# Kernel tuning notes

Hardware: AMD Instinct MI355X
Metric: run time of the kernel (lower is better)

Reference implementation:

```python
import jax, jax.numpy as jnp
import numpy as np

NQ, NL, QD, LD, H = 100000, 32, 384, 1024, 128
E, E_SEE, E_PRED = 1000000, 750000, 250000
N = NQ + NL
EPS = 1e-5


def _bn(x, g, b):
    # BatchNorm1d in training mode: biased batch statistics over node dim
    mu = x.mean(0)
    var = x.var(0)
    return g * (x - mu) * jax.lax.rsqrt(var + EPS) + b


def _general_conv(x, src, dst, ea, Wm, bm, We, be_):
    # PyG GeneralConv (heads=1, no attention, aggr='add', in==out -> identity skip)
    msg = x[src] @ Wm + bm + ea @ We + be_            # [E_see, H]
    agg = jax.ops.segment_sum(msg, dst, num_segments=N)
    return agg + x


def setup_inputs() -> dict:
    key = jax.random.key(0)
    ks = jax.random.split(key, 20)
    s = lambda fan_in: 1.0 / np.sqrt(fan_in)
    return {
        'query_features': jax.random.normal(ks[0], (NQ, QD), jnp.float32),
        'llm_features': jax.random.normal(ks[1], (NL, LD), jnp.float32),
        'edge_index': jax.random.randint(ks[2], (2, E), 0, N, jnp.int64 if jax.config.jax_enable_x64 else jnp.int32),
        'edge_mask': jax.random.randint(ks[3], (E_PRED,), 0, E),
        'edge_can_see': jax.random.randint(ks[4], (E_SEE,), 0, E),
        'edge_weight': jax.random.uniform(ks[5], (E, 1), jnp.float32),
        'Wq': jax.random.normal(ks[6], (QD, H), jnp.float32) * s(QD),
        'bq': jnp.zeros((H,), jnp.float32),
        'Wl': jax.random.normal(ks[7], (LD, H), jnp.float32) * s(LD),
        'bl': jnp.zeros((H,), jnp.float32),
        'W_em': jax.random.normal(ks[8], (1, 1), jnp.float32),
        'b_em': jnp.zeros((1,), jnp.float32),
        'W1m': jax.random.normal(ks[9], (H, H), jnp.float32) * s(H),
        'b1m': jnp.zeros((H,), jnp.float32),
        'W1e': jax.random.normal(ks[10], (1, H), jnp.float32),
        'b1e': jnp.zeros((H,), jnp.float32),
        'W2m': jax.random.normal(ks[11], (H, H), jnp.float32) * s(H),
        'b2m': jnp.zeros((H,), jnp.float32),
        'W2e': jax.random.normal(ks[12], (1, H), jnp.float32),
        'b2e': jnp.zeros((H,), jnp.float32),
        'g1': jnp.ones((H,), jnp.float32), 'beta1': jnp.zeros((H,), jnp.float32),
        'g2': jnp.ones((H,), jnp.float32), 'beta2': jnp.zeros((H,), jnp.float32),
    }


def reference(query_features, llm_features, edge_index, edge_mask, edge_can_see,
              edge_weight, Wq, bq, Wl, bl, W_em, b_em, W1m, b1m, W1e, b1e,
              W2m, b2m, W2e, b2e, g1, beta1, g2, beta2):
    lrelu = jax.nn.leaky_relu  # slope 0.01 (torch default)
    ei_mask = edge_index[:, edge_can_see]       # [2, E_see]
    ei_pred = edge_index[:, edge_mask]          # [2, E_pred]
    ew = lrelu(edge_weight[edge_can_see] @ W_em + b_em)  # [E_see, 1]
    # feature alignment
    x_ini = jnp.concatenate([query_features @ Wq + bq, llm_features @ Wl + bl], 0)  # [N, H]
    src, dst = ei_mask[0], ei_mask[1]
    x = lrelu(_bn(_general_conv(x_ini, src, dst, ew, W1m, b1m, W1e, b1e), g1, beta1))
    x = _bn(_general_conv(x, src, dst, ew, W2m, b2m, W2e, b2e), g2, beta2)
    edge_predict = jax.nn.sigmoid((x_ini[ei_pred[0]] * x[ei_pred[1]]).mean(-1))  # [E_pred]
    return edge_predict
```

## Files before the change

### kernel.cpp

```cpp
#include <hip/hip_runtime.h>
#include <math.h>

#define NQ 100000
#define NL 32
#define QD 384
#define LD 1024
#define H 128
#define E_TOT 1000000
#define E_SEE 750000
#define E_PRED 250000
#define NN (NQ + NL)
#define EPS 1e-5f

#define NB_SCAN ((NN + 255) / 256)
#define NB_GEMM ((NN + 127) / 128)
#define NB_XINI ((NQ + 127) / 128)

typedef __attribute__((ext_vector_type(8))) short short8;
typedef __attribute__((ext_vector_type(4))) short short4v;
typedef __attribute__((ext_vector_type(4))) float f32x4;

__device__ __forceinline__ unsigned short f2bf(float f) {
  unsigned int u = __builtin_bit_cast(unsigned int, f);
  u = (u + 0x7FFFu + ((u >> 16) & 1u)) >> 16;
  return (unsigned short)u;
}


__global__ void k_ew_hist(const int* __restrict__ ecs, const int* __restrict__ EI,
                          const float* __restrict__ ewt, const float* __restrict__ Wem,
                          const float* __restrict__ bem, float* __restrict__ ew,
                          int* __restrict__ cnt) {
  int e = blockIdx.x * 256 + threadIdx.x;
  if (e >= E_SEE) return;
  int idx = ecs[e];
  int d = EI[E_TOT + idx];
  atomicAdd(&cnt[d], 1);
  float w = ewt[idx] * Wem[0] + bem[0];
  ew[e] = w > 0.f ? w : 0.01f * w;
}

__global__ void k_scan_block(const int* __restrict__ cnt, int* __restrict__ bsum) {
  __shared__ int red[256];
  int i = blockIdx.x * 256 + threadIdx.x;
  red[threadIdx.x] = (i < NN) ? cnt[i] : 0;
  __syncthreads();
  for (int s = 128; s > 0; s >>= 1) {
    if (threadIdx.x < s) red[threadIdx.x] += red[threadIdx.x + s];
    __syncthreads();
  }
  if (threadIdx.x == 0) bsum[blockIdx.x] = red[0];
}

__global__ void k_scan_top(const int* __restrict__ bsum, int* __restrict__ boff) {
  __shared__ int buf[2][512];
  int t = threadIdx.x;
  int v = (t < NB_SCAN) ? bsum[t] : 0;
  buf[0][t] = v;
  __syncthreads();
  int src = 0;
  for (int d = 1; d < 512; d <<= 1) {
    int x = buf[src][t];
    if (t >= d) x += buf[src][t - d];
    buf[src ^ 1][t] = x;
    __syncthreads();
    src ^= 1;
  }
  if (t < NB_SCAN) boff[t] = buf[src][t] - v;
}

__global__ void k_scan_write(const int* __restrict__ cnt, const int* __restrict__ boff,
                             int* __restrict__ off) {
  __shared__ int buf[2][256];
  int t = threadIdx.x;
  int i = blockIdx.x * 256 + t;
  int v = (i < NN) ? cnt[i] : 0;
  buf[0][t] = v;
  __syncthreads();
  int src = 0;
  for (int d = 1; d < 256; d <<= 1) {
    int x = buf[src][t];
    if (t >= d) x += buf[src][t - d];
    buf[src ^ 1][t] = x;
    __syncthreads();
    src ^= 1;
  }
  if (i < NN) off[i] = boff[blockIdx.x] + buf[src][t] - v;
  if (i == 0) off[NN] = E_SEE;
}

__global__ void k_fill(const int* __restrict__ ecs, const int* __restrict__ EI,
                       const float* __restrict__ ew, const int* __restrict__ off,
                       int* __restrict__ cur, int* __restrict__ csr_src,
                       float* __restrict__ csr_ew) {
  int e = blockIdx.x * 256 + threadIdx.x;
  if (e >= E_SEE) return;
  int idx = ecs[e];
  int s = EI[idx];
  int d = EI[E_TOT + idx];
  int p = off[d] + atomicAdd(&cur[d], 1);
  csr_src[p] = s;
  csr_ew[p] = ew[e];
}


__global__ void k_prep(const float* __restrict__ Wq, const float* __restrict__ W1m,
                       const float* __restrict__ W2m,
                       unsigned short* __restrict__ Wqt, unsigned short* __restrict__ W1t,
                       unsigned short* __restrict__ W2t) {
  int i = blockIdx.x * 256 + threadIdx.x;
  const int tot1 = QD * H;
  const int tot2 = H * H;
  if (i < tot1) {
    int n = i / QD, k = i - n * QD;
    Wqt[i] = f2bf(Wq[(size_t)k * H + n]);
  } else if (i < tot1 + tot2) {
    int j = i - tot1;
    int n = j >> 7, k = j & 127;
    W1t[j] = f2bf(W1m[(size_t)k * H + n]);
  } else if (i < tot1 + 2 * tot2) {
    int j = i - tot1 - tot2;
    int n = j >> 7, k = j & 127;
    W2t[j] = f2bf(W2m[(size_t)k * H + n]);
  }
}


__global__ __launch_bounds__(128) void k_llm_part(const float* __restrict__ lf,
                                                  const float* __restrict__ Wl,
                                                  float* __restrict__ part) {
  int r = blockIdx.x >> 3;
  int s = blockIdx.x & 7;
  int t = threadIdx.x;
  int k0 = s * 128;
  float acc = 0.f;
#pragma unroll 4
  for (int k = 0; k < 128; k += 4) {
    float a0 = lf[(size_t)r * LD + k0 + k + 0];
    float a1 = lf[(size_t)r * LD + k0 + k + 1];
    float a2 = lf[(size_t)r * LD + k0 + k + 2];
    float a3 = lf[(size_t)r * LD + k0 + k + 3];
    acc = fmaf(a0, Wl[(size_t)(k0 + k + 0) * H + t], acc);
    acc = fmaf(a1, Wl[(size_t)(k0 + k + 1) * H + t], acc);
    acc = fmaf(a2, Wl[(size_t)(k0 + k + 2) * H + t], acc);
    acc = fmaf(a3, Wl[(size_t)(k0 + k + 3) * H + t], acc);
  }
  part[(size_t)blockIdx.x * 128 + t] = acc;
}

__global__ void k_llm_comb(const float* __restrict__ part, const float* __restrict__ bl,
                           float* __restrict__ XINI) {
  int i = blockIdx.x * 256 + threadIdx.x;
  if (i >= NL * H) return;
  int r = i >> 7, t = i & 127;
  float a = bl[t];
#pragma unroll
  for (int s = 0; s < 8; s++) a += part[(size_t)(r * 8 + s) * 128 + t];
  XINI[(size_t)(NQ + r) * H + t] = a;
}


__global__ __launch_bounds__(256) void k_xini(
    const float* __restrict__ qf, const unsigned short* __restrict__ Wqt,
    const float* __restrict__ bq, float* __restrict__ XINI) {
  __shared__ unsigned short sA[128][40];
  __shared__ unsigned short sB[128][40];
  int tid = threadIdx.x;
  int w = tid >> 6, lane = tid & 63;
  int l15 = lane & 15, quad = lane >> 4;
  int wr = (w >> 1) * 64, wc = (w & 1) * 64;
  int rowbase = blockIdx.x * 128;
  f32x4 acc[4][4];
#pragma unroll
  for (int i = 0; i < 4; i++)
#pragma unroll
    for (int j = 0; j < 4; j++) acc[i][j] = (f32x4){0.f, 0.f, 0.f, 0.f};

  int arow = tid >> 3, akc = (tid & 7) * 4;
  int bn = tid >> 2, bk8 = (tid & 3) * 8;
  float4 pa[4];
  int4 pb[2];
#pragma unroll
  for (int p = 0; p < 4; ++p) {
    int gr = rowbase + p * 32 + arow;
    pa[p] = (gr < NQ) ? *(const float4*)&qf[(size_t)gr * QD + akc]
                      : make_float4(0.f, 0.f, 0.f, 0.f);
  }
#pragma unroll
  for (int p = 0; p < 2; ++p)
    pb[p] = *(const int4*)&Wqt[(size_t)(p * 64 + bn) * QD + bk8];

  for (int step = 0; step < 12; ++step) {
    int kb = step * 32;
#pragma unroll
    for (int p = 0; p < 4; ++p) {
      short4v b;
      b.x = (short)f2bf(pa[p].x); b.y = (short)f2bf(pa[p].y);
      b.z = (short)f2bf(pa[p].z); b.w = (short)f2bf(pa[p].w);
      *(short4v*)&sA[p * 32 + arow][akc] = b;
    }
#pragma unroll
    for (int p = 0; p < 2; ++p) *(int4*)&sB[p * 64 + bn][bk8] = pb[p];
    __syncthreads();
    if (step + 1 < 12) {
      int kn = kb + 32;
#pragma unroll
      for (int p = 0; p < 4; ++p) {
        int gr = rowbase + p * 32 + arow;
        pa[p] = (gr < NQ) ? *(const float4*)&qf[(size_t)gr * QD + kn + akc]
                          : make_float4(0.f, 0.f, 0.f, 0.f);
      }
#pragma unroll
      for (int p = 0; p < 2; ++p)
        pb[p] = *(const int4*)&Wqt[(size_t)(p * 64 + bn) * QD + kn + bk8];
    }
    short8 af[4], bfr[4];
#pragma unroll
    for (int mt = 0; mt < 4; ++mt)
      af[mt] = *(const short8*)&sA[wr + mt * 16 + l15][quad * 8];
#pragma unroll
    for (int nt = 0; nt < 4; ++nt)
      bfr[nt] = *(const short8*)&sB[wc + nt * 16 + l15][quad * 8];
#pragma unroll
    for (int mt = 0; mt < 4; ++mt)
#pragma unroll
      for (int nt = 0; nt < 4; ++nt)
        acc[mt][nt] = __builtin_amdgcn_mfma_f32_16x16x32_bf16(
            af[mt], bfr[nt], acc[mt][nt], 0, 0, 0);
    __syncthreads();
  }
#pragma unroll
  for (int nt = 0; nt < 4; ++nt) {
    int col = wc + nt * 16 + l15;
    float bias = bq[col];
#pragma unroll
    for (int mt = 0; mt < 4; ++mt) {
#pragma unroll
      for (int r = 0; r < 4; ++r) {
        int n = rowbase + wr + mt * 16 + quad * 4 + r;
        if (n < NQ) XINI[(size_t)n * H + col] = acc[mt][nt][r] + bias;
      }
    }
  }
}


template <bool TRANS>
__global__ __launch_bounds__(256) void k_seg(
    const float* __restrict__ Xin, const int* __restrict__ off,
    const int* __restrict__ csr_src, const float* __restrict__ csr_ew,
    const float* __restrict__ scale, const float* __restrict__ shift,
    unsigned short* __restrict__ S16, float* __restrict__ swsum,
    float* __restrict__ degf) {
  int w = blockIdx.x * 4 + (threadIdx.x >> 6);
  if (w >= NN) return;
  int lane = threadIdx.x & 63;
  int o0 = off[w], o1 = off[w + 1];
  float ax = 1.f, ay = 1.f, bx = 0.f, by = 0.f;
  if (TRANS) {
    float2 sc = *(const float2*)&scale[lane * 2];
    float2 sh = *(const float2*)&shift[lane * 2];
    ax = sc.x; ay = sc.y; bx = sh.x; by = sh.y;
  }
  float accx = 0.f, accy = 0.f, ews = 0.f;
  for (int k = o0; k < o1; ++k) {
    int s = csr_src[k];
    float2 v = *(const float2*)&Xin[(size_t)s * H + lane * 2];
    if (TRANS) {
      float t0 = fmaf(ax, v.x, bx); v.x = t0 > 0.f ? t0 : 0.01f * t0;
      float t1 = fmaf(ay, v.y, by); v.y = t1 > 0.f ? t1 : 0.01f * t1;
    }
    accx += v.x; accy += v.y;
    ews += csr_ew[k];
  }
  unsigned int pk = ((unsigned int)f2bf(accy) << 16) | f2bf(accx);
  *(unsigned int*)&S16[(size_t)w * H + lane * 2] = pk;
  if (lane == 0) { swsum[w] = ews; degf[w] = (float)(o1 - o0); }
}


template <bool TRANS>
__global__ __launch_bounds__(256) void k_gemm(
    const unsigned short* __restrict__ S16, const float* __restrict__ Xin,
    float* __restrict__ Xout, const unsigned short* __restrict__ Wt,
    const float* __restrict__ bm, const float* __restrict__ be,
    const float* __restrict__ We,
    const float* __restrict__ scale, const float* __restrict__ shift,
    const float* __restrict__ swsum, const float* __restrict__ degf,
    float* __restrict__ partials) {
  __shared__ unsigned short sA[128][40];
  __shared__ unsigned short sB[128][40];
  __shared__ float st[2][8][128];
  int tid = threadIdx.x;
  int w = tid >> 6, lane = tid & 63;
  int l15 = lane & 15, quad = lane >> 4;
  int wr = (w >> 1) * 64, wc = (w & 1) * 64;
  int rowbase = blockIdx.x * 128;
  f32x4 acc[4][4];
#pragma unroll
  for (int i = 0; i < 4; i++)
#pragma unroll
    for (int j = 0; j < 4; j++) acc[i][j] = (f32x4){0.f, 0.f, 0.f, 0.f};

  int arow = tid >> 1, ah = (tid & 1) * 16;
  int4 pa[2], pb[2];
  {
    int gr = rowbase + arow;
    if (gr < NN) {
      pa[0] = *(const int4*)&S16[(size_t)gr * H + ah];
      pa[1] = *(const int4*)&S16[(size_t)gr * H + ah + 8];
    } else {
      pa[0] = make_int4(0, 0, 0, 0); pa[1] = make_int4(0, 0, 0, 0);
    }
    pb[0] = *(const int4*)&Wt[(size_t)arow * H + ah];
    pb[1] = *(const int4*)&Wt[(size_t)arow * H + ah + 8];
  }
  for (int step = 0; step < 4; ++step) {
    *(int4*)&sA[arow][ah] = pa[0];
    *(int4*)&sA[arow][ah + 8] = pa[1];
    *(int4*)&sB[arow][ah] = pb[0];
    *(int4*)&sB[arow][ah + 8] = pb[1];
    __syncthreads();
    if (step + 1 < 4) {
      int kn = (step + 1) * 32;
      int gr = rowbase + arow;
      if (gr < NN) {
        pa[0] = *(const int4*)&S16[(size_t)gr * H + kn + ah];
        pa[1] = *(const int4*)&S16[(size_t)gr * H + kn + ah + 8];
      } else {
        pa[0] = make_int4(0, 0, 0, 0); pa[1] = make_int4(0, 0, 0, 0);
      }
      pb[0] = *(const int4*)&Wt[(size_t)arow * H + kn + ah];
      pb[1] = *(const int4*)&Wt[(size_t)arow * H + kn + ah + 8];
    }
    short8 af[4], bfr[4];
#pragma unroll
    for (int mt = 0; mt < 4; ++mt)
      af[mt] = *(const short8*)&sA[wr + mt * 16 + l15][quad * 8];
#pragma unroll
    for (int nt = 0; nt < 4; ++nt)
      bfr[nt] = *(const short8*)&sB[wc + nt * 16 + l15][quad * 8];
#pragma unroll
    for (int mt = 0; mt < 4; ++mt)
#pragma unroll
      for (int nt = 0; nt < 4; ++nt)
        acc[mt][nt] = __builtin_amdgcn_mfma_f32_16x16x32_bf16(
            af[mt], bfr[nt], acc[mt][nt], 0, 0, 0);
    __syncthreads();
  }
  int col4[4];
  float cb4[4], we4[4], sc4[4], sh4[4], ps[4], pq[4];
#pragma unroll
  for (int nt = 0; nt < 4; ++nt) {
    int col = wc + nt * 16 + l15;
    col4[nt] = col;
    cb4[nt] = bm[col] + be[col];
    we4[nt] = We[col];
    if (TRANS) { sc4[nt] = scale[col]; sh4[nt] = shift[col]; }
    ps[nt] = 0.f; pq[nt] = 0.f;
  }
#pragma unroll
  for (int mt = 0; mt < 4; ++mt) {
#pragma unroll
    for (int r = 0; r < 4; ++r) {
      int n = rowbase + wr + mt * 16 + quad * 4 + r;
      if (n < NN) {
        float dg = degf[n], sw = swsum[n];
#pragma unroll
        for (int nt = 0; nt < 4; ++nt) {
          float rr = Xin[(size_t)n * H + col4[nt]];
          if (TRANS) {
            float t = fmaf(sc4[nt], rr, sh4[nt]);
            rr = t > 0.f ? t : 0.01f * t;
          }
          float o = acc[mt][nt][r] + dg * cb4[nt] + sw * we4[nt] + rr;
          Xout[(size_t)n * H + col4[nt]] = o;
          ps[nt] += o; pq[nt] += o * o;
        }
      }
    }
  }
  int slot = (w >> 1) * 4 + quad;
#pragma unroll
  for (int nt = 0; nt < 4; ++nt) {
    st[0][slot][col4[nt]] = ps[nt];
    st[1][slot][col4[nt]] = pq[nt];
  }
  __syncthreads();
  int plane = tid >> 7, col = tid & 127;
  float s = 0.f;
#pragma unroll
  for (int y = 0; y < 8; y++) s += st[plane][y][col];
  partials[(size_t)blockIdx.x * 256 + tid] = s;
}


__global__ __launch_bounds__(256) void k_bnstats(
    const float* __restrict__ partials, const float* __restrict__ g,
    const float* __restrict__ beta, float* __restrict__ scale,
    float* __restrict__ shift) {
  __shared__ float rs[256], rq[256];
  int j = blockIdx.x;
  int t = threadIdx.x;
  float as = 0.f, aq = 0.f;
  for (int b = t; b < NB_GEMM; b += 256) {
    as += partials[(size_t)b * 256 + j];
    aq += partials[(size_t)b * 256 + 128 + j];
  }
  rs[t] = as; rq[t] = aq;
  __syncthreads();
  for (int s = 128; s > 0; s >>= 1) {
    if (t < s) { rs[t] += rs[t + s]; rq[t] += rq[t + s]; }
    __syncthreads();
  }
  if (t == 0) {
    float mean = rs[0] / (float)NN;
    float var = rq[0] / (float)NN - mean * mean;
    float a = g[j] * rsqrtf(var + EPS);
    scale[j] = a;
    shift[j] = beta[j] - mean * a;
  }
}


__global__ __launch_bounds__(256) void k_pred(
    const int* __restrict__ emask, const int* __restrict__ EI,
    const float* __restrict__ XINI, const float* __restrict__ X,
    const float* __restrict__ scale, const float* __restrict__ shift,
    float* __restrict__ out) {
  int i = blockIdx.x * 4 + (threadIdx.x >> 6);
  if (i >= E_PRED) return;
  int lane = threadIdx.x & 63;
  int m = emask[i];
  int p0 = EI[m];
  int p1 = EI[E_TOT + m];
  float2 a = *(const float2*)&XINI[(size_t)p0 * H + lane * 2];
  float2 b = *(const float2*)&X[(size_t)p1 * H + lane * 2];
  float2 sc = *(const float2*)&scale[lane * 2];
  float2 sh = *(const float2*)&shift[lane * 2];
  float v = a.x * fmaf(sc.x, b.x, sh.x) + a.y * fmaf(sc.y, b.y, sh.y);
#pragma unroll
  for (int mm = 32; mm > 0; mm >>= 1) v += __shfl_xor(v, mm, 64);
  if (lane == 0) out[i] = 1.f / (1.f + expf(-v * (1.f / 128.f)));
}


extern "C" void kernel_launch(void* const* d_in, const int* in_sizes, int n_in,
                              void* d_out, int out_size, void* d_ws, size_t ws_size,
                              hipStream_t stream) {
  const float* qf    = (const float*)d_in[0];
  const float* lf    = (const float*)d_in[1];
  const int*   EI    = (const int*)d_in[2];
  const int*   emask = (const int*)d_in[3];
  const int*   ecs   = (const int*)d_in[4];
  const float* ewt   = (const float*)d_in[5];
  const float* Wq    = (const float*)d_in[6];
  const float* bq    = (const float*)d_in[7];
  const float* Wl    = (const float*)d_in[8];
  const float* bl    = (const float*)d_in[9];
  const float* Wem   = (const float*)d_in[10];
  const float* bem   = (const float*)d_in[11];
  const float* W1m   = (const float*)d_in[12];
  const float* b1m   = (const float*)d_in[13];
  const float* W1e   = (const float*)d_in[14];
  const float* b1e   = (const float*)d_in[15];
  const float* W2m   = (const float*)d_in[16];
  const float* b2m   = (const float*)d_in[17];
  const float* W2e   = (const float*)d_in[18];
  const float* b2e   = (const float*)d_in[19];
  const float* g1    = (const float*)d_in[20];
  const float* beta1 = (const float*)d_in[21];
  const float* g2    = (const float*)d_in[22];
  const float* beta2 = (const float*)d_in[23];
  float* out = (float*)d_out;

  char* p = (char*)d_ws;
  auto alloc = [&](size_t bytes) -> void* {
    void* r = (void*)p;
    p += (bytes + 255) & ~(size_t)255;
    return r;
  };
  float* XINI    = (float*)alloc((size_t)NN * H * 4);
  float* X       = (float*)alloc((size_t)NN * H * 4);
  unsigned short* S16 = (unsigned short*)alloc((size_t)NN * H * 2);
  float* ew      = (float*)alloc((size_t)E_SEE * 4);
  float* csr_ew  = (float*)alloc((size_t)E_SEE * 4);
  int*   csr_src = (int*)alloc((size_t)E_SEE * 4);
  int*   cnt     = (int*)alloc((size_t)NN * 4);
  int*   off     = (int*)alloc((size_t)(NN + 1) * 4);
  int*   cur     = (int*)alloc((size_t)NN * 4);
  int*   bsum    = (int*)alloc((size_t)NB_SCAN * 4);
  int*   boff    = (int*)alloc((size_t)NB_SCAN * 4);
  float* swsum   = (float*)alloc((size_t)NN * 4);
  float* degf    = (float*)alloc((size_t)NN * 4);
  float* partials= (float*)alloc((size_t)NB_GEMM * 256 * 4);
  float* scale1  = (float*)alloc(128 * 4);
  float* shift1  = (float*)alloc(128 * 4);
  float* scale2  = (float*)alloc(128 * 4);
  float* shift2  = (float*)alloc(128 * 4);
  unsigned short* Wqt = (unsigned short*)alloc((size_t)QD * H * 2);
  unsigned short* W1t = (unsigned short*)alloc((size_t)H * H * 2);
  unsigned short* W2t = (unsigned short*)alloc((size_t)H * H * 2);
  float* llmpart = (float*)alloc((size_t)NL * 8 * H * 4);

  hipMemsetAsync(cnt, 0, (size_t)NN * 4, stream);
  hipMemsetAsync(cur, 0, (size_t)NN * 4, stream);

  int ebl = (E_SEE + 255) / 256;
  k_prep<<<320, 256, 0, stream>>>(Wq, W1m, W2m, Wqt, W1t, W2t);
  k_ew_hist<<<ebl, 256, 0, stream>>>(ecs, EI, ewt, Wem, bem, ew, cnt);
  k_scan_block<<<NB_SCAN, 256, 0, stream>>>(cnt, bsum);
  k_scan_top<<<1, 512, 0, stream>>>(bsum, boff);
  k_scan_write<<<NB_SCAN, 256, 0, stream>>>(cnt, boff, off);
  k_fill<<<ebl, 256, 0, stream>>>(ecs, EI, ew, off, cur, csr_src, csr_ew);

  k_llm_part<<<NL * 8, 128, 0, stream>>>(lf, Wl, llmpart);
  k_llm_comb<<<(NL * H + 255) / 256, 256, 0, stream>>>(llmpart, bl, XINI);
  k_xini<<<NB_XINI, 256, 0, stream>>>(qf, Wqt, bq, XINI);

  int segbl = (NN + 3) / 4;
  k_seg<false><<<segbl, 256, 0, stream>>>(XINI, off, csr_src, csr_ew,
                                          nullptr, nullptr, S16, swsum, degf);
  k_gemm<false><<<NB_GEMM, 256, 0, stream>>>(S16, XINI, X, W1t, b1m, b1e, W1e,
                                             nullptr, nullptr, swsum, degf, partials);
  k_bnstats<<<H, 256, 0, stream>>>(partials, g1, beta1, scale1, shift1);
  k_seg<true><<<segbl, 256, 0, stream>>>(X, off, csr_src, csr_ew,
                                         scale1, shift1, S16, swsum, degf);
  k_gemm<true><<<NB_GEMM, 256, 0, stream>>>(S16, X, X, W2t, b2m, b2e, W2e,
                                            scale1, shift1, swsum, degf, partials);
  k_bnstats<<<H, 256, 0, stream>>>(partials, g2, beta2, scale2, shift2);
  int pbl = (E_PRED + 3) / 4;
  k_pred<<<pbl, 256, 0, stream>>>(emask, EI, XINI, X, scale2, shift2, out);
}
```

Baseline: 722.1 us.

## Drop LDS staging in query projection GEMM, load MFMA fragments from global

```diff
diff --git a/kernel.cpp b/kernel.cpp
--- a/kernel.cpp
+++ b/kernel.cpp
@@ -19,6 +19,7 @@
 typedef __attribute__((ext_vector_type(8))) short short8;
 typedef __attribute__((ext_vector_type(4))) short short4v;
 typedef __attribute__((ext_vector_type(4))) float f32x4;
+typedef __attribute__((ext_vector_type(4))) unsigned int uint4v;
 
 __device__ __forceinline__ unsigned short f2bf(float f) {
   unsigned int u = __builtin_bit_cast(unsigned int, f);
@@ -160,85 +161,80 @@
 }
 
 
-__global__ __launch_bounds__(256) void k_xini(
+__global__ __launch_bounds__(256, 3) void k_xini(
     const float* __restrict__ qf, const unsigned short* __restrict__ Wqt,
     const float* __restrict__ bq, float* __restrict__ XINI) {
-  __shared__ unsigned short sA[128][40];
-  __shared__ unsigned short sB[128][40];
   int tid = threadIdx.x;
-  int w = tid >> 6, lane = tid & 63;
+  int lane = tid & 63;
+  int w = tid >> 6;
   int l15 = lane & 15, quad = lane >> 4;
-  int wr = (w >> 1) * 64, wc = (w & 1) * 64;
-  int rowbase = blockIdx.x * 128;
-  f32x4 acc[4][4];
-#pragma unroll
-  for (int i = 0; i < 4; i++)
-#pragma unroll
-    for (int j = 0; j < 4; j++) acc[i][j] = (f32x4){0.f, 0.f, 0.f, 0.f};
-
-  int arow = tid >> 3, akc = (tid & 7) * 4;
-  int bn = tid >> 2, bk8 = (tid & 3) * 8;
-  float4 pa[4];
-  int4 pb[2];
-#pragma unroll
-  for (int p = 0; p < 4; ++p) {
-    int gr = rowbase + p * 32 + arow;
-    pa[p] = (gr < NQ) ? *(const float4*)&qf[(size_t)gr * QD + akc]
-                      : make_float4(0.f, 0.f, 0.f, 0.f);
-  }
-#pragma unroll
-  for (int p = 0; p < 2; ++p)
-    pb[p] = *(const int4*)&Wqt[(size_t)(p * 64 + bn) * QD + bk8];
+  int rowbase = blockIdx.x * 128 + w * 32;
+
+  f32x4 acc[2][8];
+#pragma unroll
+  for (int i = 0; i < 2; ++i)
+#pragma unroll
+    for (int j = 0; j < 8; ++j) acc[i][j] = (f32x4){0.f, 0.f, 0.f, 0.f};
+
+  int r0 = rowbase + l15;
+  int r1 = rowbase + 16 + l15;
+  const float* rp0 = qf + (size_t)r0 * QD;
+  const float* rp1 = qf + (size_t)r1 * QD;
+  bool v0 = r0 < NQ, v1 = r1 < NQ;
+  const unsigned short* bp = Wqt + (size_t)l15 * QD + quad * 8;
+
+  float4 pf[2][2];
+  {
+    int ko = quad * 8;
+    pf[0][0] = v0 ? *(const float4*)(rp0 + ko) : make_float4(0.f, 0.f, 0.f, 0.f);
+    pf[0][1] = v0 ? *(const float4*)(rp0 + ko + 4) : make_float4(0.f, 0.f, 0.f, 0.f);
+    pf[1][0] = v1 ? *(const float4*)(rp1 + ko) : make_float4(0.f, 0.f, 0.f, 0.f);
+    pf[1][1] = v1 ? *(const float4*)(rp1 + ko + 4) : make_float4(0.f, 0.f, 0.f, 0.f);
+  }
 
   for (int step = 0; step < 12; ++step) {
     int kb = step * 32;
-#pragma unroll
-    for (int p = 0; p < 4; ++p) {
-      short4v b;
-      b.x = (short)f2bf(pa[p].x); b.y = (short)f2bf(pa[p].y);
-      b.z = (short)f2bf(pa[p].z); b.w = (short)f2bf(pa[p].w);
-      *(short4v*)&sA[p * 32 + arow][akc] = b;
-    }
-#pragma unroll
-    for (int p = 0; p < 2; ++p) *(int4*)&sB[p * 64 + bn][bk8] = pb[p];
-    __syncthreads();
+    short8 bfr[8];
+#pragma unroll
+    for (int nt = 0; nt < 8; ++nt)
+      bfr[nt] = *(const short8*)(bp + (size_t)nt * 16 * QD + kb);
+    short8 af[2];
+#pragma unroll
+    for (int mt = 0; mt < 2; ++mt) {
+      uint4v pk;
+      pk.x = ((unsigned int)f2bf(pf[mt][0].y) << 16) | f2bf(pf[mt][0].x);
+      pk.y = ((unsigned int)f2bf(pf[mt][0].w) << 16) | f2bf(pf[mt][0].z);
+      pk.z = ((unsigned int)f2bf(pf[mt][1].y) << 16) | f2bf(pf[mt][1].x);
+      pk.w = ((unsigned int)f2bf(pf[mt][1].w) << 16) | f2bf(pf[mt][1].z);
+      af[mt] = __builtin_bit_cast(short8, pk);
+    }
     if (step + 1 < 12) {
-      int kn = kb + 32;
-#pragma unroll
-      for (int p = 0; p < 4; ++p) {
-        int gr = rowbase + p * 32 + arow;
-        pa[p] = (gr < NQ) ? *(const float4*)&qf[(size_t)gr * QD + kn + akc]
-                          : make_float4(0.f, 0.f, 0.f, 0.f);
-      }
-#pragma unroll
-      for (int p = 0; p < 2; ++p)
-        pb[p] = *(const int4*)&Wqt[(size_t)(p * 64 + bn) * QD + kn + bk8];
-    }
-    short8 af[4], bfr[4];
-#pragma unroll
-    for (int mt = 0; mt < 4; ++mt)
-      af[mt] = *(const short8*)&sA[wr + mt * 16 + l15][quad * 8];
-#pragma unroll
-    for (int nt = 0; nt < 4; ++nt)
-      bfr[nt] = *(const short8*)&sB[wc + nt * 16 + l15][quad * 8];
-#pragma unroll
-    for (int mt = 0; mt < 4; ++mt)
-#pragma unroll
-      for (int nt = 0; nt < 4; ++nt)
+      int ko = kb + 32 + quad * 8;
+      pf[0][0] = v0 ? *(const float4*)(rp0 + ko) : make_float4(0.f, 0.f, 0.f, 0.f);
+      pf[0][1] = v0 ? *(const float4*)(rp0 + ko + 4) : make_float4(0.f, 0.f, 0.f, 0.f);
+      pf[1][0] = v1 ? *(const float4*)(rp1 + ko) : make_float4(0.f, 0.f, 0.f, 0.f);
+      pf[1][1] = v1 ? *(const float4*)(rp1 + ko + 4) : make_float4(0.f, 0.f, 0.f, 0.f);
+    }
+#pragma unroll
+    for (int mt = 0; mt < 2; ++mt)
+#pragma unroll
+      for (int nt = 0; nt < 8; ++nt)
         acc[mt][nt] = __builtin_amdgcn_mfma_f32_16x16x32_bf16(
             af[mt], bfr[nt], acc[mt][nt], 0, 0, 0);
-    __syncthreads();
-  }
-#pragma unroll
-  for (int nt = 0; nt < 4; ++nt) {
-    int col = wc + nt * 16 + l15;
-    float bias = bq[col];
-#pragma unroll
-    for (int mt = 0; mt < 4; ++mt) {
-#pragma unroll
-      for (int r = 0; r < 4; ++r) {
-        int n = rowbase + wr + mt * 16 + quad * 4 + r;
-        if (n < NQ) XINI[(size_t)n * H + col] = acc[mt][nt][r] + bias;
+  }
+
+  float bias[8];
+#pragma unroll
+  for (int nt = 0; nt < 8; ++nt) bias[nt] = bq[nt * 16 + l15];
+#pragma unroll
+  for (int mt = 0; mt < 2; ++mt) {
+#pragma unroll
+    for (int r = 0; r < 4; ++r) {
+      int n = rowbase + mt * 16 + quad * 4 + r;
+      if (n < NQ) {
+#pragma unroll
+        for (int nt = 0; nt < 8; ++nt)
+          XINI[(size_t)n * H + nt * 16 + l15] = acc[mt][nt][r] + bias[nt];
       }
     }
   }
```

Result: no change. 728.7 us (+0.9%).
